# Performance work log

Hardware: AMD Instinct MI355X
Metric: run time of the kernel (lower is better)

Reference implementation:

```python
import jax, jax.numpy as jnp
import numpy as np

IN_FEATURES = 4096
OUT_FEATURES = 4096
INPUT_SCALE = 0.05
OUTPUT_SCALE = 0.05


def setup_inputs() -> dict:
    key = jax.random.key(0)
    k_x, k_w, k_ws = jax.random.split(key, 3)
    # int8 activations (already quantized upstream in W8A8 pipeline)
    x = jax.random.randint(k_x, (4, 2048, IN_FEATURES), -128, 128, dtype=jnp.int32).astype(jnp.int8)
    # simulate per-tensor absmax quantization of an fp32 weight
    w_fp = jax.random.normal(k_w, (OUT_FEATURES, IN_FEATURES), dtype=jnp.float32) * 0.02
    weight_scale = jnp.max(jnp.abs(w_fp)) / 127.0
    w_int8 = jnp.clip(jnp.round(w_fp / weight_scale), -128, 127).astype(jnp.int8)
    weight = w_int8.T  # stored as [in_features, out_features], matching int8_weight.t()
    a = jnp.array([[INPUT_SCALE / OUTPUT_SCALE]], dtype=jnp.float32)
    b = jnp.reshape(weight_scale.astype(jnp.float32), (1, 1))
    return {"x": x, "weight": weight, "a": a, "b": b}


def reference(x, weight, a, b):
    # round and saturate back to int8 (output dtype == x.dtype == int8).
    x_shape = x.shape
    x2 = x.reshape(-1, x_shape[-1]).astype(jnp.int32)          # [N, D]
    acc = jnp.matmul(x2, weight.astype(jnp.int32))             # [N, O] int32 accum
    scale = (a * b)[0, 0]                                      # alpha = in_scale*w_scale/out_scale
    y = jnp.clip(jnp.round(acc.astype(jnp.float32) * scale), -128.0, 127.0).astype(jnp.int8)
    return y.reshape(*x_shape[:-1], -1)
```

## Files before the change

### kernel.cpp

```cpp
#include <hip/hip_runtime.h>
#include <stdint.h>

typedef __attribute__((ext_vector_type(4))) int int4v;
typedef __attribute__((ext_vector_type(16))) int int16v;
typedef __attribute__((ext_vector_type(4))) uint32_t uint4v;

#define M_DIM 8192
#define N_DIM 4096
#define K_DIM 4096


__global__ void pack_a_perm(const int* __restrict__ x, uint4v* __restrict__ a8) {
    const int g = blockIdx.x * blockDim.x + threadIdx.x;
    const int w0 = (g & 3) * 4;
    const int chunk = g >> 2;
    const int* base = x + (size_t)chunk * 64;
    int4v L[4];
#pragma unroll
    for (int j = 0; j < 4; ++j) L[j] = *(const int4v*)(base + j * 16 + w0);
    uint4v outv;
#pragma unroll
    for (int wi = 0; wi < 4; ++wi) {
        outv[wi] = (uint32_t)(L[0][wi] & 0xff) | ((uint32_t)(L[1][wi] & 0xff) << 8) |
                   ((uint32_t)(L[2][wi] & 0xff) << 16) | ((uint32_t)(L[3][wi] & 0xff) << 24);
    }
    a8[g] = outv;
}

__global__ void transpose_b_perm(const int* __restrict__ w, int8_t* __restrict__ bt) {
    const int t = threadIdx.x;
    const int kt = blockIdx.y * 64;
    const int n0 = blockIdx.x * 64;
    const int c4 = t & 3;
    const int n = t >> 2;
    const int w0 = c4 * 4;
    const int* col = w + (size_t)kt * N_DIM + n0 + n;
    uint4v outv;
#pragma unroll
    for (int wi = 0; wi < 4; ++wi) {
        uint32_t p = 0;
#pragma unroll
        for (int j = 0; j < 4; ++j) {
            uint32_t b = (uint32_t)(col[(size_t)(w0 + wi + 16 * j) * N_DIM] & 0xff);
            p |= b << (8 * j);
        }
        outv[wi] = p;
    }
    *(uint4v*)&bt[(size_t)(n0 + n) * K_DIM + kt + w0 * 4] = outv;
}

__device__ inline void async16(const void* g, void* l) {
    __builtin_amdgcn_global_load_lds(
        (const __attribute__((address_space(1))) uint32_t*)g,
        (__attribute__((address_space(3))) uint32_t*)l, 16, 0, 0);
}

__global__ void __launch_bounds__(256)
gemm_kernel(const int8_t* __restrict__ A, const int8_t* __restrict__ Bt,
            const float* __restrict__ pa, const float* __restrict__ pb,
            int* __restrict__ out) {
    __shared__ int8_t smem[32768];
    int8_t* As = smem;
    int8_t* Bs = smem + 16384;

    const int t = threadIdx.x;
    const int lane = t & 63;
    const int wave = t >> 6;
    const int m0 = blockIdx.y * 128;
    const int n0 = blockIdx.x * 128;
    const int wm = (wave >> 1) * 64;
    const int wn = (wave & 1) * 64;
    const float scale = pa[0] * pb[0];

    int16v acc[2][2];
#pragma unroll
    for (int i = 0; i < 2; ++i)
#pragma unroll
        for (int j = 0; j < 2; ++j)
#pragma unroll
            for (int r = 0; r < 16; ++r) acc[i][j][r] = 0;

    const int srow = lane >> 3;
    const int sslot = lane & 7;

    const int fm0 = wm + (lane & 31);
    const int fn0 = wn + (lane & 31);
    const int fg = lane >> 5;

    for (int kt = 0; kt < K_DIM; kt += 128) {
        __syncthreads();
#pragma unroll
        for (int s = 0; s < 4; ++s) {
            const int base_row = wave * 8 + s * 32;
            const int row = base_row + srow;
            const int cA = (sslot ^ (row & 7)) * 16;
            async16(A + (size_t)(m0 + row) * K_DIM + kt + cA, As + base_row * 128);
            async16(Bt + (size_t)(n0 + row) * K_DIM + kt + cA, Bs + base_row * 128);
        }
        __syncthreads();

#pragma unroll
        for (int ks = 0; ks < 4; ++ks) {
            int4v af[2], bf[2];
            const int cc = ks * 2 + fg;
#pragma unroll
            for (int i = 0; i < 2; ++i) {
                const int ra = fm0 + i * 32;
                af[i] = *(const int4v*)&As[ra * 128 + ((cc ^ (ra & 7)) * 16)];
                const int rb = fn0 + i * 32;
                bf[i] = *(const int4v*)&Bs[rb * 128 + ((cc ^ (rb & 7)) * 16)];
            }
#pragma unroll
            for (int i = 0; i < 2; ++i)
#pragma unroll
                for (int j = 0; j < 2; ++j)
                    acc[i][j] = __builtin_amdgcn_mfma_i32_32x32x32_i8(af[i], bf[j],
                                                                       acc[i][j], 0, 0, 0);
        }
    }

    const int col = lane & 31;
    const int rbase = (lane >> 5) * 4;
#pragma unroll
    for (int i = 0; i < 2; ++i)
#pragma unroll
        for (int j = 0; j < 2; ++j)
#pragma unroll
            for (int r = 0; r < 16; ++r) {
                const int rowf = rbase + (r & 3) + 8 * (r >> 2);
                float v = (float)acc[i][j][r] * scale;
                v = rintf(v);
                v = fminf(127.f, fmaxf(-128.f, v));
                out[(size_t)(m0 + wm + i * 32 + rowf) * N_DIM +
                    (n0 + wn + j * 32 + col)] = (int)v;
            }
}

extern "C" void kernel_launch(void* const* d_in, const int* in_sizes, int n_in,
                              void* d_out, int out_size, void* d_ws, size_t ws_size,
                              hipStream_t stream) {
    const int* x = (const int*)d_in[0];
    const int* w = (const int*)d_in[1];
    const float* pa = (const float*)d_in[2];
    const float* pb = (const float*)d_in[3];
    int* out = (int*)d_out;

    int8_t* a8 = (int8_t*)d_ws;
    int8_t* bt8 = a8 + (size_t)M_DIM * K_DIM;

    const int nwords_a = M_DIM * K_DIM / 16;
    pack_a_perm<<<nwords_a / 256, 256, 0, stream>>>(x, (uint4v*)a8);
    transpose_b_perm<<<dim3(N_DIM / 64, K_DIM / 64), 256, 0, stream>>>(w, bt8);
    gemm_kernel<<<dim3(N_DIM / 128, M_DIM / 128), 256, 0, stream>>>(a8, bt8, pa, pb, out);
}
```

Measured before the change: 409.6 us.

## Use 256x256 tiles with double-buffered LDS ping-pong pipeline and XCD-aware block remap

Replaces the 128x128 single-buffered GEMM with a 512-thread 256x256-tile kernel. It uses two 64KB LDS buffers and interleaves async global-to-LDS loads of the next K tile with MFMA phases, using explicit s_barrier, waitcnt and setprio scheduling. Blocks are remapped so that consecutive workgroups on the same XCD share tiles. This aims to hide global memory latency and raise data reuse per block, at the cost of 128KB of LDS per block, which limits occupancy, and of fragile hand-placed synchronization.

```diff
diff --git a/kernel.cpp b/kernel.cpp
--- a/kernel.cpp
+++ b/kernel.cpp
@@ -55,85 +55,147 @@
         (__attribute__((address_space(3))) uint32_t*)l, 16, 0, 0);
 }
 
-__global__ void __launch_bounds__(256)
+__global__ void __launch_bounds__(512, 2)
 gemm_kernel(const int8_t* __restrict__ A, const int8_t* __restrict__ Bt,
             const float* __restrict__ pa, const float* __restrict__ pb,
             int* __restrict__ out) {
-    __shared__ int8_t smem[32768];
-    int8_t* As = smem;
-    int8_t* Bs = smem + 16384;
+    __shared__ int8_t smem[131072];
 
     const int t = threadIdx.x;
     const int lane = t & 63;
     const int wave = t >> 6;
-    const int m0 = blockIdx.y * 128;
-    const int n0 = blockIdx.x * 128;
-    const int wm = (wave >> 1) * 64;
-    const int wn = (wave & 1) * 64;
+
+    int wg = (int)blockIdx.x;
+    wg = (wg & 7) * (512 / 8) + (wg >> 3);
+    const int bx = wg & 15;
+    const int by = wg >> 4;
+    const int m0 = by * 256;
+    const int n0 = bx * 256;
+
+    const int wm = (wave >> 2) * 128;
+    const int wn = (wave & 3) * 64;
     const float scale = pa[0] * pb[0];
 
-    int16v acc[2][2];
-#pragma unroll
-    for (int i = 0; i < 2; ++i)
+    const int srow8 = wave * 8 + (lane >> 3);
+    const int gcol = ((lane & 7) ^ (srow8 & 7)) * 16;
+    const int8_t* pA = A + (size_t)(m0 + srow8) * K_DIM + gcol;
+    const int8_t* pB = Bt + (size_t)(n0 + srow8) * K_DIM + gcol;
+
+    const int ra0 = wm + (lane & 31);
+    const int rb0 = wn + (lane & 31);
+    const int rx7 = lane & 7;
+    const int hl = lane >> 5;
+
+    int16v acc[4][2];
+#pragma unroll
+    for (int mi = 0; mi < 4; ++mi)
 #pragma unroll
         for (int j = 0; j < 2; ++j)
 #pragma unroll
-            for (int r = 0; r < 16; ++r) acc[i][j][r] = 0;
-
-    const int srow = lane >> 3;
-    const int sslot = lane & 7;
-
-    const int fm0 = wm + (lane & 31);
-    const int fn0 = wn + (lane & 31);
-    const int fg = lane >> 5;
-
-    for (int kt = 0; kt < K_DIM; kt += 128) {
-        __syncthreads();
-#pragma unroll
-        for (int s = 0; s < 4; ++s) {
-            const int base_row = wave * 8 + s * 32;
-            const int row = base_row + srow;
-            const int cA = (sslot ^ (row & 7)) * 16;
-            async16(A + (size_t)(m0 + row) * K_DIM + kt + cA, As + base_row * 128);
-            async16(Bt + (size_t)(n0 + row) * K_DIM + kt + cA, Bs + base_row * 128);
-        }
-        __syncthreads();
-
-#pragma unroll
-        for (int ks = 0; ks < 4; ++ks) {
-            int4v af[2], bf[2];
-            const int cc = ks * 2 + fg;
-#pragma unroll
-            for (int i = 0; i < 2; ++i) {
-                const int ra = fm0 + i * 32;
-                af[i] = *(const int4v*)&As[ra * 128 + ((cc ^ (ra & 7)) * 16)];
-                const int rb = fn0 + i * 32;
-                bf[i] = *(const int4v*)&Bs[rb * 128 + ((cc ^ (rb & 7)) * 16)];
-            }
-#pragma unroll
-            for (int i = 0; i < 2; ++i)
-#pragma unroll
-                for (int j = 0; j < 2; ++j)
-                    acc[i][j] = __builtin_amdgcn_mfma_i32_32x32x32_i8(af[i], bf[j],
-                                                                       acc[i][j], 0, 0, 0);
-        }
+            for (int r = 0; r < 16; ++r) acc[mi][j][r] = 0;
+
+    int4v af[2][2], bf[2][2];
+
+#define STAGE_A(c, kt, buf) async16(pA + (size_t)(c) * 64 * K_DIM + (kt), \
+                                    smem + (buf) * 65536 + ((c) * 64 + wave * 8) * 128)
+#define STAGE_B(c, kt, buf) async16(pB + (size_t)(c) * 64 * K_DIM + (kt), \
+                                    smem + (buf) * 65536 + 32768 + ((c) * 64 + wave * 8) * 128)
+
+#define PH_READ(BUF, KH, MH, READB) do {                                          \
+        const int abase_ = (BUF) * 65536;                                         \
+        if (READB) {                                                              \
+            _Pragma("unroll")                                                     \
+            for (int ks = 0; ks < 2; ++ks) {                                      \
+                const int off_ = ((((KH) * 2 + ks) * 2 + hl) ^ rx7) << 4;         \
+                bf[0][ks] = *(const int4v*)&smem[abase_ + 32768 + rb0 * 128 + off_]; \
+                bf[1][ks] = *(const int4v*)&smem[abase_ + 32768 + (rb0 + 32) * 128 + off_]; \
+            }                                                                     \
+        }                                                                         \
+        _Pragma("unroll")                                                         \
+        for (int ks = 0; ks < 2; ++ks) {                                          \
+            const int off_ = ((((KH) * 2 + ks) * 2 + hl) ^ rx7) << 4;             \
+            af[0][ks] = *(const int4v*)&smem[abase_ + (ra0 + (MH) * 64) * 128 + off_]; \
+            af[1][ks] = *(const int4v*)&smem[abase_ + (ra0 + (MH) * 64 + 32) * 128 + off_]; \
+        }                                                                         \
+    } while (0)
+
+#define PH_TAIL(MH, ENDWAIT) do {                                                 \
+        __builtin_amdgcn_sched_barrier(0);                                        \
+        __builtin_amdgcn_s_barrier();                                             \
+        asm volatile("s_waitcnt lgkmcnt(0)");                                     \
+        __builtin_amdgcn_sched_barrier(0);                                        \
+        __builtin_amdgcn_s_setprio(1);                                            \
+        _Pragma("unroll")                                                         \
+        for (int ks = 0; ks < 2; ++ks)                                            \
+            _Pragma("unroll")                                                     \
+            for (int i = 0; i < 2; ++i)                                           \
+                _Pragma("unroll")                                                 \
+                for (int j = 0; j < 2; ++j)                                       \
+                    acc[(MH) * 2 + i][j] = __builtin_amdgcn_mfma_i32_32x32x32_i8( \
+                        af[i][ks], bf[j][ks], acc[(MH) * 2 + i][j], 0, 0, 0);     \
+        __builtin_amdgcn_s_setprio(0);                                            \
+        if (ENDWAIT) asm volatile("s_waitcnt vmcnt(2)");                          \
+        __builtin_amdgcn_s_barrier();                                             \
+    } while (0)
+
+    STAGE_A(0, 0, 0); STAGE_A(2, 0, 0);
+    STAGE_B(0, 0, 0); STAGE_B(1, 0, 0);
+    STAGE_B(2, 0, 0); STAGE_B(3, 0, 0);
+    STAGE_A(1, 0, 0); STAGE_A(3, 0, 0);
+    asm volatile("s_waitcnt vmcnt(2)");
+    __builtin_amdgcn_s_barrier();
+
+#pragma unroll 1
+    for (int t2 = 0; t2 < 32; t2 += 2) {
+        const int kt1 = t2 * 128 + 128;
+        const int kt2 = (t2 * 128 + 256) & (K_DIM - 1);
+        PH_READ(0, 0, 0, 1);
+        STAGE_A(0, kt1, 1); STAGE_A(2, kt1, 1);
+        PH_TAIL(0, 1);
+        PH_READ(0, 0, 1, 0);
+        STAGE_B(0, kt1, 1); STAGE_B(1, kt1, 1);
+        PH_TAIL(1, 0);
+        PH_READ(0, 1, 0, 1);
+        STAGE_B(2, kt1, 1); STAGE_B(3, kt1, 1);
+        PH_TAIL(0, 0);
+        PH_READ(0, 1, 1, 0);
+        STAGE_A(1, kt1, 1); STAGE_A(3, kt1, 1);
+        PH_TAIL(1, 1);
+        PH_READ(1, 0, 0, 1);
+        STAGE_A(0, kt2, 0); STAGE_A(2, kt2, 0);
+        PH_TAIL(0, 1);
+        PH_READ(1, 0, 1, 0);
+        STAGE_B(0, kt2, 0); STAGE_B(1, kt2, 0);
+        PH_TAIL(1, 0);
+        PH_READ(1, 1, 0, 1);
+        STAGE_B(2, kt2, 0); STAGE_B(3, kt2, 0);
+        PH_TAIL(0, 0);
+        PH_READ(1, 1, 1, 0);
+        STAGE_A(1, kt2, 0); STAGE_A(3, kt2, 0);
+        PH_TAIL(1, 1);
     }
+
+    asm volatile("s_waitcnt vmcnt(0)");
 
     const int col = lane & 31;
     const int rbase = (lane >> 5) * 4;
 #pragma unroll
-    for (int i = 0; i < 2; ++i)
+    for (int mi = 0; mi < 4; ++mi)
 #pragma unroll
         for (int j = 0; j < 2; ++j)
 #pragma unroll
             for (int r = 0; r < 16; ++r) {
                 const int rowf = rbase + (r & 3) + 8 * (r >> 2);
-                float v = (float)acc[i][j][r] * scale;
+                float v = (float)acc[mi][j][r] * scale;
                 v = rintf(v);
                 v = fminf(127.f, fmaxf(-128.f, v));
-                out[(size_t)(m0 + wm + i * 32 + rowf) * N_DIM +
+                out[(size_t)(m0 + wm + mi * 32 + rowf) * N_DIM +
                     (n0 + wn + j * 32 + col)] = (int)v;
             }
+#undef STAGE_A
+#undef STAGE_B
+#undef PH_READ
+#undef PH_TAIL
 }
 
 extern "C" void kernel_launch(void* const* d_in, const int* in_sizes, int n_in,
@@ -151,5 +213,5 @@
     const int nwords_a = M_DIM * K_DIM / 16;
     pack_a_perm<<<nwords_a / 256, 256, 0, stream>>>(x, (uint4v*)a8);
     transpose_b_perm<<<dim3(N_DIM / 64, K_DIM / 64), 256, 0, stream>>>(w, bt8);
-    gemm_kernel<<<dim3(N_DIM / 128, M_DIM / 128), 256, 0, stream>>>(a8, bt8, pa, pb, out);
-}
+    gemm_kernel<<<dim3(512), dim3(512), 0, stream>>>(a8, bt8, pa, pb, out);
+}
```

Result: faster. 400.4 us (-2.3%).

## Rewrite int8 GEMM with 256x256 tiles and 4-stage async LDS pipeline

Applied to the files above, without the earlier changes.

Restructures the main GEMM kernel to use 256x256 block tiles with 512 threads (8 waves, each computing 128x64), a 4-buffer LDS ring fed by global_load_lds, and a software-pipelined loop. The loop double-buffers register fragments, places explicit waitcnt and barriers, and raises wave priority around the MFMA bursts. Blocks are remapped through a swizzled 1D grid to improve L2 locality. The goal is to raise data reuse per tile and hide global-load latency behind MFMA work. In exchange it uses 128KB of LDS per block, and the hand-tuned waitcnt counts and pipeline depth are fragile.

```diff
diff --git a/kernel.cpp b/kernel.cpp
--- a/kernel.cpp
+++ b/kernel.cpp
@@ -55,85 +55,129 @@
         (__attribute__((address_space(3))) uint32_t*)l, 16, 0, 0);
 }
 
-__global__ void __launch_bounds__(256)
+#define SB() __builtin_amdgcn_sched_barrier(0)
+#define BAR() do { SB(); __builtin_amdgcn_s_barrier(); SB(); } while (0)
+
+__global__ void __launch_bounds__(512, 2)
 gemm_kernel(const int8_t* __restrict__ A, const int8_t* __restrict__ Bt,
             const float* __restrict__ pa, const float* __restrict__ pb,
             int* __restrict__ out) {
-    __shared__ int8_t smem[32768];
-    int8_t* As = smem;
-    int8_t* Bs = smem + 16384;
+    __shared__ int8_t smem[131072];
 
     const int t = threadIdx.x;
     const int lane = t & 63;
     const int wave = t >> 6;
-    const int m0 = blockIdx.y * 128;
-    const int n0 = blockIdx.x * 128;
-    const int wm = (wave >> 1) * 64;
-    const int wn = (wave & 1) * 64;
+
+    int wg = (int)blockIdx.x;
+    wg = (wg & 7) * 64 + (wg >> 3);
+    const int bx = wg & 15;
+    const int by = wg >> 4;
+    const int m0 = by * 256;
+    const int n0 = bx * 256;
+
+    const int wm = (wave >> 2) * 128;
+    const int wn = (wave & 3) * 64;
     const float scale = pa[0] * pb[0];
 
-    int16v acc[2][2];
+    const int srow = wave * 16 + (lane >> 2);
+    const int gx = ((lane & 3) ^ (srow & 3)) * 16;
+    const int8_t* pA0 = A + (size_t)(m0 + srow) * K_DIM + gx;
+    const int8_t* pA1 = A + (size_t)(m0 + 128 + srow) * K_DIM + gx;
+    const int8_t* pB0 = Bt + (size_t)(n0 + srow) * K_DIM + gx;
+    const int8_t* pB1 = Bt + (size_t)(n0 + 128 + srow) * K_DIM + gx;
+    const int ldsA0 = wave * 1024;
+    const int ldsA1 = 8192 + wave * 1024;
+    const int ldsB0 = 16384 + wave * 1024;
+    const int ldsB1 = 16384 + 8192 + wave * 1024;
+
+    const int rl = lane & 31;
+    const int hl = lane >> 5;
+    const int xl = lane & 3;
+    const int koffE = (hl ^ xl) * 16;
+    const int koffO = ((2 + hl) ^ xl) * 16;
+    const int raBase = (wm + rl) * 64;
+    const int rbBase = 16384 + (wn + rl) * 64;
+
+    int16v acc[4][2];
 #pragma unroll
-    for (int i = 0; i < 2; ++i)
+    for (int mi = 0; mi < 4; ++mi)
 #pragma unroll
         for (int j = 0; j < 2; ++j)
 #pragma unroll
-            for (int r = 0; r < 16; ++r) acc[i][j][r] = 0;
+            for (int r = 0; r < 16; ++r) acc[mi][j][r] = 0;
 
-    const int srow = lane >> 3;
-    const int sslot = lane & 7;
+    int4v afE[4], bfE[2], afO[4], bfO[2];
 
-    const int fm0 = wm + (lane & 31);
-    const int fn0 = wn + (lane & 31);
-    const int fg = lane >> 5;
+#define STAGE(TT) do {                                                   \
+        const int b_ = ((TT) & 3) * 32768;                               \
+        const int kt_ = ((TT) & 63) * 64;        \
+        async16(pA0 + kt_, smem + b_ + ldsA0);                           \
+        async16(pA1 + kt_, smem + b_ + ldsA1);                           \
+        async16(pB0 + kt_, smem + b_ + ldsB0);                           \
+        async16(pB1 + kt_, smem + b_ + ldsB1);                           \
+    } while (0)
 
-    for (int kt = 0; kt < K_DIM; kt += 128) {
-        __syncthreads();
-#pragma unroll
-        for (int s = 0; s < 4; ++s) {
-            const int base_row = wave * 8 + s * 32;
-            const int row = base_row + srow;
-            const int cA = (sslot ^ (row & 7)) * 16;
-            async16(A + (size_t)(m0 + row) * K_DIM + kt + cA, As + base_row * 128);
-            async16(Bt + (size_t)(n0 + row) * K_DIM + kt + cA, Bs + base_row * 128);
-        }
-        __syncthreads();
+#define RD_SET(AF, BF, BUF, KOFF) do {                                   \
+        const int ab_ = (BUF) * 32768;                                   \
+        AF[0] = *(const int4v*)&smem[ab_ + raBase + 0 * 2048 + (KOFF)];  \
+        AF[1] = *(const int4v*)&smem[ab_ + raBase + 1 * 2048 + (KOFF)];  \
+        AF[2] = *(const int4v*)&smem[ab_ + raBase + 2 * 2048 + (KOFF)];  \
+        AF[3] = *(const int4v*)&smem[ab_ + raBase + 3 * 2048 + (KOFF)];  \
+        BF[0] = *(const int4v*)&smem[ab_ + rbBase + 0 * 2048 + (KOFF)];  \
+        BF[1] = *(const int4v*)&smem[ab_ + rbBase + 1 * 2048 + (KOFF)];  \
+    } while (0)
 
-#pragma unroll
-        for (int ks = 0; ks < 4; ++ks) {
-            int4v af[2], bf[2];
-            const int cc = ks * 2 + fg;
-#pragma unroll
-            for (int i = 0; i < 2; ++i) {
-                const int ra = fm0 + i * 32;
-                af[i] = *(const int4v*)&As[ra * 128 + ((cc ^ (ra & 7)) * 16)];
-                const int rb = fn0 + i * 32;
-                bf[i] = *(const int4v*)&Bs[rb * 128 + ((cc ^ (rb & 7)) * 16)];
-            }
-#pragma unroll
-            for (int i = 0; i < 2; ++i)
-#pragma unroll
-                for (int j = 0; j < 2; ++j)
-                    acc[i][j] = __builtin_amdgcn_mfma_i32_32x32x32_i8(af[i], bf[j],
-                                                                       acc[i][j], 0, 0, 0);
-        }
+#define MM(AF, BF) do {                                                  \
+        __builtin_amdgcn_s_setprio(1);                                   \
+        _Pragma("unroll")                                                \
+        for (int mi = 0; mi < 4; ++mi)                                   \
+            _Pragma("unroll")                                            \
+            for (int j = 0; j < 2; ++j)                                  \
+                acc[mi][j] = __builtin_amdgcn_mfma_i32_32x32x32_i8(      \
+                    AF[mi], BF[j], acc[mi][j], 0, 0, 0);                 \
+        __builtin_amdgcn_s_setprio(0);                                   \
+    } while (0)
+
+    STAGE(0); STAGE(1); STAGE(2);
+    asm volatile("s_waitcnt vmcnt(8)" ::: "memory");
+    BAR();
+    RD_SET(afE, bfE, 0, koffE);
+
+#pragma unroll 1
+    for (int tt = 0; tt < 64; ++tt) {
+        STAGE(tt + 3);
+        RD_SET(afO, bfO, tt & 3, koffO);
+        SB();
+        MM(afE, bfE);
+        SB();
+        asm volatile("s_waitcnt vmcnt(8)" ::: "memory");
+        BAR();
+        RD_SET(afE, bfE, (tt + 1) & 3, koffE);
+        SB();
+        MM(afO, bfO);
+        BAR();
     }
+
+    asm volatile("s_waitcnt vmcnt(0) lgkmcnt(0)" ::: "memory");
 
     const int col = lane & 31;
     const int rbase = (lane >> 5) * 4;
 #pragma unroll
-    for (int i = 0; i < 2; ++i)
+    for (int mi = 0; mi < 4; ++mi)
 #pragma unroll
         for (int j = 0; j < 2; ++j)
 #pragma unroll
             for (int r = 0; r < 16; ++r) {
                 const int rowf = rbase + (r & 3) + 8 * (r >> 2);
-                float v = (float)acc[i][j][r] * scale;
+                float v = (float)acc[mi][j][r] * scale;
                 v = rintf(v);
                 v = fminf(127.f, fmaxf(-128.f, v));
-                out[(size_t)(m0 + wm + i * 32 + rowf) * N_DIM +
+                out[(size_t)(m0 + wm + mi * 32 + rowf) * N_DIM +
                     (n0 + wn + j * 32 + col)] = (int)v;
             }
+#undef STAGE
+#undef RD_SET
+#undef MM
 }
 
 extern "C" void kernel_launch(void* const* d_in, const int* in_sizes, int n_in,
@@ -151,5 +195,5 @@
     const int nwords_a = M_DIM * K_DIM / 16;
     pack_a_perm<<<nwords_a / 256, 256, 0, stream>>>(x, (uint4v*)a8);
     transpose_b_perm<<<dim3(N_DIM / 64, K_DIM / 64), 256, 0, stream>>>(w, bt8);
-    gemm_kernel<<<dim3(N_DIM / 128, M_DIM / 128), 256, 0, stream>>>(a8, bt8, pa, pb, out);
+    gemm_kernel<<<dim3(512), dim3(512), 0, stream>>>(a8, bt8, pa, pb, out);
 }
```

New measurement: 416.4 us. No clear change (+1.7%).
